# Kernel tuning notes

Hardware: AMD Instinct MI355X
Metric: run time of the kernel (lower is better)

The kernel has to match this reference:

```python
import jax, jax.numpy as jnp
import numpy as np

N_NODES = 100000
N_EDGES = 1600000
IN_F = 64
OUT_F = 40
K_HOPS = 3
N_CLUSTERS = 10000


def setup_inputs() -> dict:
    key = jax.random.key(0)
    k1, k2, k3, k4 = jax.random.split(key, 4)
    x = jax.random.normal(k1, (N_NODES, IN_F), dtype=jnp.float32)
    edge_index = jax.random.randint(k2, (2, N_EDGES), 0, N_NODES, dtype=jnp.int32)
    cluster_index = jax.random.randint(k3, (N_NODES,), 0, N_CLUSTERS, dtype=jnp.int32)
    W = jax.random.normal(k4, (OUT_F, IN_F), dtype=jnp.float32) * (1.0 / np.sqrt(IN_F))
    b = jnp.zeros((OUT_F,), dtype=jnp.float32)
    return {"x": x, "edge_index": edge_index, "cluster_index": cluster_index,
            "num_clusters": N_CLUSTERS, "W": W, "b": b}


def reference(x, edge_index, cluster_index, num_clusters, W, b):
    N = x.shape[0]
    self_loop = jnp.arange(N, dtype=edge_index.dtype)
    row = jnp.concatenate([edge_index[0], self_loop])  # target nodes
    col = jnp.concatenate([edge_index[1], self_loop])  # source nodes
    ones = jnp.ones(row.shape[0], dtype=x.dtype)
    deg = jax.ops.segment_sum(ones, row, num_segments=N)
    dinv = jax.lax.rsqrt(jnp.maximum(deg, 1.0))
    norm = dinv[row] * dinv[col]  # [E+N] symmetric GCN normalization
    # K-hop propagation: x <- D^{-1/2} (A+I) D^{-1/2} x, K times
    for _ in range(K_HOPS):
        x = jax.ops.segment_sum(x[col] * norm[:, None], row, num_segments=N)
    # cluster/compress: segment-mean of node features per cluster -> [C, F]
    cnt = jax.ops.segment_sum(jnp.ones(N, dtype=x.dtype), cluster_index,
                              num_segments=num_clusters)
    xc = jax.ops.segment_sum(x, cluster_index, num_segments=num_clusters)
    xc = xc / jnp.maximum(cnt, 1.0)[:, None]
    # dense linear on compressed rows, then reconstruct (gather back)
    h = xc @ W.T + b  # [C, OUT_F]
    out = h[cluster_index]  # [N, OUT_F]
    # original module computes log_softmax into a local `out` but returns x
    return out
```

## Files before the change

### kernel.cpp

```cpp
#include <hip/hip_runtime.h>

#define N_NODES    100000
#define N_EDGES    1600000
#define IN_F       64
#define OUT_F      40
#define N_CLUSTERS 10000

#define BUCK_SHIFT 7
#define BROWS      128
#define NBUCK      ((N_NODES + BROWS - 1) >> BUCK_SHIFT)
#define CAP        2560
#define TILE_E     4096
#define EPT        (TILE_E / 256)

typedef _Float16 half_t;
typedef _Float16 half4_t __attribute__((ext_vector_type(4)));

__global__ __launch_bounds__(256) void bin_scatter_kernel(
        const int* __restrict__ rows, const int* __restrict__ cols,
        int* __restrict__ bcursor, unsigned* __restrict__ bins) {
    __shared__ uint2 se[TILE_E];
    __shared__ int lh[NBUCK];
    __shared__ int lsc[NBUCK];
    __shared__ int lb[NBUCK];
    __shared__ int sc[256];
    int t = threadIdx.x;
    for (int i = t; i < NBUCK; i += 256) lh[i] = 0;
    __syncthreads();
    int e0 = blockIdx.x * TILE_E;
    int r[EPT], c[EPT], rk[EPT];
    #pragma unroll
    for (int k = 0; k < EPT; ++k) {
        int e = e0 + t + k * 256;
        if (e < N_EDGES) {
            r[k] = rows[e]; c[k] = cols[e];
            rk[k] = atomicAdd(&lh[r[k] >> BUCK_SHIFT], 1);
        } else r[k] = -1;
    }
    __syncthreads();
    int b4 = t * 4;
    int a0 = (b4 + 0 < NBUCK) ? lh[b4 + 0] : 0;
    int a1 = (b4 + 1 < NBUCK) ? lh[b4 + 1] : 0;
    int a2 = (b4 + 2 < NBUCK) ? lh[b4 + 2] : 0;
    int a3 = (b4 + 3 < NBUCK) ? lh[b4 + 3] : 0;
    int thr = a0 + a1 + a2 + a3;
    sc[t] = thr;
    __syncthreads();
    for (int off = 1; off < 256; off <<= 1) {
        int a = (t >= off) ? sc[t - off] : 0;
        __syncthreads();
        sc[t] += a;
        __syncthreads();
    }
    int ex = sc[t] - thr;
    if (b4 + 0 < NBUCK) { lsc[b4 + 0] = ex;                lb[b4 + 0] = a0 ? atomicAdd(&bcursor[b4 + 0], a0) : 0; }
    if (b4 + 1 < NBUCK) { lsc[b4 + 1] = ex + a0;           lb[b4 + 1] = a1 ? atomicAdd(&bcursor[b4 + 1], a1) : 0; }
    if (b4 + 2 < NBUCK) { lsc[b4 + 2] = ex + a0 + a1;      lb[b4 + 2] = a2 ? atomicAdd(&bcursor[b4 + 2], a2) : 0; }
    if (b4 + 3 < NBUCK) { lsc[b4 + 3] = ex + a0 + a1 + a2; lb[b4 + 3] = a3 ? atomicAdd(&bcursor[b4 + 3], a3) : 0; }
    __syncthreads();
    #pragma unroll
    for (int k = 0; k < EPT; ++k) {
        if (r[k] >= 0) {
            int bu = r[k] >> BUCK_SHIFT;
            se[lsc[bu] + rk[k]] = make_uint2((unsigned)r[k], (unsigned)c[k]);
        }
    }
    __syncthreads();
    #pragma unroll
    for (int k = 0; k < EPT; ++k) {
        int idx = k * 256 + t;
        if (e0 + idx < N_EDGES) {
            uint2 u = se[idx];
            int bu = (int)(u.x >> BUCK_SHIFT);
            int pos = lb[bu] + (idx - lsc[bu]);
            if (pos < CAP)
                bins[(size_t)bu * CAP + pos] = ((u.x & (BROWS - 1)) << 17) | u.y;
        }
    }
}

__global__ __launch_bounds__(256) void csr_build_kernel(
        const unsigned* __restrict__ bins, const int* __restrict__ bcnt,
        int* __restrict__ csr_col, uint2* __restrict__ rowinfo,
        float* __restrict__ dinv, const int* __restrict__ cl,
        int* __restrict__ ccnt) {
    __shared__ int lcnt[BROWS];
    __shared__ int gbeg[BROWS];
    __shared__ int sc[BROWS];
    int b = blockIdx.x, t = threadIdx.x;
    int n = min(bcnt[b], CAP);
    const unsigned* eb = bins + (size_t)b * CAP;
    if (t < BROWS) lcnt[t] = 0;
    __syncthreads();
    for (int i = t; i < n; i += 256) atomicAdd(&lcnt[eb[i] >> 17], 1);
    __syncthreads();
    int v = (t < BROWS) ? lcnt[t] : 0;
    if (t < BROWS) sc[t] = v;
    __syncthreads();
    for (int off = 1; off < BROWS; off <<= 1) {
        int a = (t >= off && t < BROWS) ? sc[t - off] : 0;
        __syncthreads();
        if (t < BROWS) sc[t] += a;
        __syncthreads();
    }
    if (t < BROWS) {
        int beg = b * CAP + sc[t] - v;
        gbeg[t] = beg;
        int grow = (b << BUCK_SHIFT) + t;
        if (grow < N_NODES) {
            rowinfo[grow] = make_uint2((unsigned)beg, (unsigned)v);
            dinv[grow] = rsqrtf((float)(v + 1));
            atomicAdd(&ccnt[cl[grow]], 1);
        }
        lcnt[t] = 0;
    }
    __syncthreads();
    for (int i = t; i < n; i += 256) {
        unsigned u = eb[i];
        int lrow = (int)(u >> 17);
        int pos = atomicAdd(&lcnt[lrow], 1);
        csr_col[gbeg[lrow] + pos] = (int)(u & 0x1FFFFu);
    }
}

__global__ __launch_bounds__(256, 8) void prologue_kernel(
        const float4* __restrict__ x4, const float* __restrict__ W,
        const float* __restrict__ dinv, half_t* __restrict__ z0) {
    __shared__ float Ws[OUT_F * 65];
    int t = threadIdx.x;
    for (int i = t; i < OUT_F * IN_F; i += 256)
        Ws[(i >> 6) * 65 + (i & 63)] = W[i];
    __syncthreads();
    int idx = blockIdx.x * 256 + t;
    if (idx >= N_NODES * OUT_F) return;
    int node = idx / OUT_F;
    int o = idx - node * OUT_F;
    const float4* xr = x4 + node * 16;
    const float* wr = Ws + o * 65;
    float acc = 0.f;
    #pragma unroll
    for (int k4 = 0; k4 < 16; ++k4) {
        float4 v = xr[k4];
        acc += v.x * wr[k4 * 4 + 0] + v.y * wr[k4 * 4 + 1]
             + v.z * wr[k4 * 4 + 2] + v.w * wr[k4 * 4 + 3];
    }
    z0[idx] = (half_t)(acc * dinv[node]);
}

template<int FINAL>
__global__ __launch_bounds__(256, 8) void hop40_kernel(
        const half_t* __restrict__ zin, half_t* __restrict__ zout,
        const uint2* __restrict__ rowinfo, const int* __restrict__ csr_col,
        const float* __restrict__ dinv, const int* __restrict__ cl,
        float* __restrict__ xc) {
    __shared__ half4_t srow[160];
    int t = threadIdx.x;
    int w = t >> 6;
    int lane = t & 63;
    int slot = lane / 10;
    int ql = lane - slot * 10;
    int slotj = (slot < 6) ? slot : 1000;
    int nb = blockIdx.x << 4;
    #pragma unroll
    for (int i = 0; i < 4; ++i) {
        int node = nb + (w << 2) + i;
        uint2 ri = rowinfo[node];
        int beg = (int)ri.x;
        int end = beg + (int)ri.y;
        float4 acc = make_float4(0.f, 0.f, 0.f, 0.f);
        if (slot == 0) {
            half4_t v = ((const half4_t*)(zin + (size_t)node * OUT_F))[ql];
            acc.x = (float)v.x; acc.y = (float)v.y; acc.z = (float)v.z; acc.w = (float)v.w;
        }
        for (int base = beg; base < end; base += 64) {
            int idx = base + lane;
            int cv = (idx < end) ? csr_col[idx] : 0;
            int lim = min(64, end - base);
            int gmax = (lim + 23) / 24;
            for (int g = 0; g < gmax; ++g) {
                int j0 = g * 24 + slotj;
                int c0 = __shfl(cv, (j0     ) & 63);
                int c1 = __shfl(cv, (j0 +  6) & 63);
                int c2 = __shfl(cv, (j0 + 12) & 63);
                int c3 = __shfl(cv, (j0 + 18) & 63);
                half4_t v0 = ((const half4_t*)(zin + (size_t)c0 * OUT_F))[ql];
                half4_t v1 = ((const half4_t*)(zin + (size_t)c1 * OUT_F))[ql];
                half4_t v2 = ((const half4_t*)(zin + (size_t)c2 * OUT_F))[ql];
                half4_t v3 = ((const half4_t*)(zin + (size_t)c3 * OUT_F))[ql];
                float m0 = (j0      < lim) ? 1.f : 0.f;
                float m1 = (j0 +  6 < lim) ? 1.f : 0.f;
                float m2 = (j0 + 12 < lim) ? 1.f : 0.f;
                float m3 = (j0 + 18 < lim) ? 1.f : 0.f;
                acc.x += m0 * (float)v0.x; acc.y += m0 * (float)v0.y;
                acc.z += m0 * (float)v0.z; acc.w += m0 * (float)v0.w;
                acc.x += m1 * (float)v1.x; acc.y += m1 * (float)v1.y;
                acc.z += m1 * (float)v1.z; acc.w += m1 * (float)v1.w;
                acc.x += m2 * (float)v2.x; acc.y += m2 * (float)v2.y;
                acc.z += m2 * (float)v2.z; acc.w += m2 * (float)v2.w;
                acc.x += m3 * (float)v3.x; acc.y += m3 * (float)v3.y;
                acc.z += m3 * (float)v3.z; acc.w += m3 * (float)v3.w;
            }
        }
        float4 t1;
        t1.x = __shfl(acc.x, (lane + 30) & 63); t1.y = __shfl(acc.y, (lane + 30) & 63);
        t1.z = __shfl(acc.z, (lane + 30) & 63); t1.w = __shfl(acc.w, (lane + 30) & 63);
        if (lane < 30) { acc.x += t1.x; acc.y += t1.y; acc.z += t1.z; acc.w += t1.w; }
        float4 t2, t3;
        t2.x = __shfl(acc.x, (lane + 10) & 63); t2.y = __shfl(acc.y, (lane + 10) & 63);
        t2.z = __shfl(acc.z, (lane + 10) & 63); t2.w = __shfl(acc.w, (lane + 10) & 63);
        t3.x = __shfl(acc.x, (lane + 20) & 63); t3.y = __shfl(acc.y, (lane + 20) & 63);
        t3.z = __shfl(acc.z, (lane + 20) & 63); t3.w = __shfl(acc.w, (lane + 20) & 63);
        if (lane < 10) {
            acc.x += t2.x + t3.x; acc.y += t2.y + t3.y;
            acc.z += t2.z + t3.z; acc.w += t2.w + t3.w;
            float d = dinv[node];
            if (FINAL) {
                float* p = xc + cl[node] * OUT_F + ql * 4;
                atomicAdd(p + 0, acc.x * d); atomicAdd(p + 1, acc.y * d);
                atomicAdd(p + 2, acc.z * d); atomicAdd(p + 3, acc.w * d);
            } else {
                float s = d * d;
                half4_t o;
                o.x = (half_t)(acc.x * s); o.y = (half_t)(acc.y * s);
                o.z = (half_t)(acc.z * s); o.w = (half_t)(acc.w * s);
                srow[((w << 2) + i) * 10 + ql] = o;
            }
        }
    }
    if (!FINAL) {
        __syncthreads();
        if (t < 160) ((half4_t*)zout)[(size_t)blockIdx.x * 160 + t] = srow[t];
    }
}

__global__ void epilogue_kernel(const float4* __restrict__ xc4, const int* __restrict__ ccnt,
                                const float4* __restrict__ b4, const int* __restrict__ cl,
                                float4* __restrict__ out4) {
    int i = blockIdx.x * 256 + threadIdx.x;
    if (i >= N_NODES * (OUT_F / 4)) return;
    int node = i / 10;
    int q = i - node * 10;
    int c = cl[node];
    float inv = 1.0f / fmaxf((float)ccnt[c], 1.0f);
    float4 v = xc4[c * 10 + q];
    float4 bb = b4[q];
    v.x = v.x * inv + bb.x; v.y = v.y * inv + bb.y;
    v.z = v.z * inv + bb.z; v.w = v.w * inv + bb.w;
    out4[i] = v;
}

extern "C" void kernel_launch(void* const* d_in, const int* in_sizes, int n_in,
                              void* d_out, int out_size, void* d_ws, size_t ws_size,
                              hipStream_t stream) {
    const float* x    = (const float*)d_in[0];
    const int*   rows = (const int*)d_in[1];
    const int*   cols = (const int*)d_in[1] + N_EDGES;
    const int*   cl   = (const int*)d_in[2];
    const float* W    = (const float*)d_in[4];
    const float* b    = (const float*)d_in[5];
    float* out = (float*)d_out;

    size_t off = 0;
    auto alloc = [&](size_t elems) -> void* {
        void* p = (char*)d_ws + off * 4;
        off += (elems + 63) & ~(size_t)63;
        return p;
    };
    int*   ccnt    = (int*)alloc(N_CLUSTERS);
    float* xc_sum  = (float*)alloc((size_t)N_CLUSTERS * OUT_F);
    int*   bcursor = (int*)alloc(NBUCK);
    size_t zero_elems = off;
    float* dinv      = (float*)alloc(N_NODES);
    uint2* rowinfo   = (uint2*)alloc((size_t)N_NODES * 2);
    int*   csr_col   = (int*)alloc((size_t)NBUCK * CAP);
    unsigned* bins   = (unsigned*)alloc((size_t)NBUCK * CAP);
    half_t* bufA     = (half_t*)alloc((size_t)N_NODES * OUT_F / 2);
    half_t* bufB     = (half_t*)alloc((size_t)N_NODES * OUT_F / 2);
    (void)ws_size; (void)in_sizes; (void)n_in; (void)out_size;

    hipMemsetAsync(d_ws, 0, zero_elems * 4, stream);

    const int TB = (N_EDGES + TILE_E - 1) / TILE_E;
    const int HB = N_NODES / 16;

    bin_scatter_kernel<<<TB, 256, 0, stream>>>(rows, cols, bcursor, bins);
    csr_build_kernel<<<NBUCK, 256, 0, stream>>>(bins, bcursor, csr_col, rowinfo,
                                                dinv, cl, ccnt);

    prologue_kernel<<<(N_NODES * OUT_F + 255) / 256, 256, 0, stream>>>(
        (const float4*)x, W, dinv, bufA);

    hop40_kernel<0><<<HB, 256, 0, stream>>>(bufA, bufB, rowinfo, csr_col, dinv, cl, xc_sum);
    hop40_kernel<0><<<HB, 256, 0, stream>>>(bufB, bufA, rowinfo, csr_col, dinv, cl, xc_sum);
    hop40_kernel<1><<<HB, 256, 0, stream>>>(bufA, (half_t*)nullptr, rowinfo, csr_col, dinv, cl, xc_sum);

    epilogue_kernel<<<(N_NODES * (OUT_F / 4) + 255) / 256, 256, 0, stream>>>(
        (const float4*)xc_sum, ccnt, (const float4*)b, cl, (float4*)out);
}
```

Baseline: 335.5 us.

## Split 40-wide features into two 20-wide halves propagated separately

The feature matrix is stored as two separate 20-column fp16 arrays, and the three-hop propagation runs twice, once per half. The goal is a 2MB working set per hop that fits better in L2/MALL for the random gathers, and 12 edges processed in parallel per wavefront instead of 6. The cost is launching six hop kernels instead of three, reading the CSR twice as often, and a deeper shuffle reduction. Column indices are now loaded with nontemporal hints.

After: 457.8 us. 1.36x slower.

```diff
diff --git a/kernel.cpp b/kernel.cpp
--- a/kernel.cpp
+++ b/kernel.cpp
@@ -125,7 +125,8 @@
 
 __global__ __launch_bounds__(256, 8) void prologue_kernel(
         const float4* __restrict__ x4, const float* __restrict__ W,
-        const float* __restrict__ dinv, half_t* __restrict__ z0) {
+        const float* __restrict__ dinv, half_t* __restrict__ zlo,
+        half_t* __restrict__ zhi) {
     __shared__ float Ws[OUT_F * 65];
     int t = threadIdx.x;
     for (int i = t; i < OUT_F * IN_F; i += 256)
@@ -144,22 +145,24 @@
         acc += v.x * wr[k4 * 4 + 0] + v.y * wr[k4 * 4 + 1]
              + v.z * wr[k4 * 4 + 2] + v.w * wr[k4 * 4 + 3];
     }
-    z0[idx] = (half_t)(acc * dinv[node]);
+    half_t h = (half_t)(acc * dinv[node]);
+    if (o < 20) zlo[node * 20 + o]      = h;
+    else        zhi[node * 20 + o - 20] = h;
 }
 
 template<int FINAL>
-__global__ __launch_bounds__(256, 8) void hop40_kernel(
+__global__ __launch_bounds__(256, 8) void hop20_kernel(
         const half_t* __restrict__ zin, half_t* __restrict__ zout,
         const uint2* __restrict__ rowinfo, const int* __restrict__ csr_col,
         const float* __restrict__ dinv, const int* __restrict__ cl,
-        float* __restrict__ xc) {
-    __shared__ half4_t srow[160];
+        float* __restrict__ xc, int dbase) {
+    __shared__ half4_t srow[80];
     int t = threadIdx.x;
     int w = t >> 6;
     int lane = t & 63;
-    int slot = lane / 10;
-    int ql = lane - slot * 10;
-    int slotj = (slot < 6) ? slot : 1000;
+    int slot = lane / 5;
+    int ql = lane - slot * 5;
+    int slotj = (slot < 12) ? slot : 1000;
     int nb = blockIdx.x << 4;
     #pragma unroll
     for (int i = 0; i < 4; ++i) {
@@ -169,28 +172,28 @@
         int end = beg + (int)ri.y;
         float4 acc = make_float4(0.f, 0.f, 0.f, 0.f);
         if (slot == 0) {
-            half4_t v = ((const half4_t*)(zin + (size_t)node * OUT_F))[ql];
+            half4_t v = ((const half4_t*)(zin + (size_t)node * 20))[ql];
             acc.x = (float)v.x; acc.y = (float)v.y; acc.z = (float)v.z; acc.w = (float)v.w;
         }
         for (int base = beg; base < end; base += 64) {
             int idx = base + lane;
-            int cv = (idx < end) ? csr_col[idx] : 0;
+            int cv = (idx < end) ? __builtin_nontemporal_load(csr_col + idx) : 0;
             int lim = min(64, end - base);
-            int gmax = (lim + 23) / 24;
+            int gmax = (lim + 47) / 48;
             for (int g = 0; g < gmax; ++g) {
-                int j0 = g * 24 + slotj;
+                int j0 = g * 48 + slotj;
                 int c0 = __shfl(cv, (j0     ) & 63);
-                int c1 = __shfl(cv, (j0 +  6) & 63);
-                int c2 = __shfl(cv, (j0 + 12) & 63);
-                int c3 = __shfl(cv, (j0 + 18) & 63);
-                half4_t v0 = ((const half4_t*)(zin + (size_t)c0 * OUT_F))[ql];
-                half4_t v1 = ((const half4_t*)(zin + (size_t)c1 * OUT_F))[ql];
-                half4_t v2 = ((const half4_t*)(zin + (size_t)c2 * OUT_F))[ql];
-                half4_t v3 = ((const half4_t*)(zin + (size_t)c3 * OUT_F))[ql];
+                int c1 = __shfl(cv, (j0 + 12) & 63);
+                int c2 = __shfl(cv, (j0 + 24) & 63);
+                int c3 = __shfl(cv, (j0 + 36) & 63);
+                half4_t v0 = ((const half4_t*)(zin + (size_t)c0 * 20))[ql];
+                half4_t v1 = ((const half4_t*)(zin + (size_t)c1 * 20))[ql];
+                half4_t v2 = ((const half4_t*)(zin + (size_t)c2 * 20))[ql];
+                half4_t v3 = ((const half4_t*)(zin + (size_t)c3 * 20))[ql];
                 float m0 = (j0      < lim) ? 1.f : 0.f;
-                float m1 = (j0 +  6 < lim) ? 1.f : 0.f;
-                float m2 = (j0 + 12 < lim) ? 1.f : 0.f;
-                float m3 = (j0 + 18 < lim) ? 1.f : 0.f;
+                float m1 = (j0 + 12 < lim) ? 1.f : 0.f;
+                float m2 = (j0 + 24 < lim) ? 1.f : 0.f;
+                float m3 = (j0 + 36 < lim) ? 1.f : 0.f;
                 acc.x += m0 * (float)v0.x; acc.y += m0 * (float)v0.y;
                 acc.z += m0 * (float)v0.z; acc.w += m0 * (float)v0.w;
                 acc.x += m1 * (float)v1.x; acc.y += m1 * (float)v1.y;
@@ -205,17 +208,21 @@
         t1.x = __shfl(acc.x, (lane + 30) & 63); t1.y = __shfl(acc.y, (lane + 30) & 63);
         t1.z = __shfl(acc.z, (lane + 30) & 63); t1.w = __shfl(acc.w, (lane + 30) & 63);
         if (lane < 30) { acc.x += t1.x; acc.y += t1.y; acc.z += t1.z; acc.w += t1.w; }
-        float4 t2, t3;
-        t2.x = __shfl(acc.x, (lane + 10) & 63); t2.y = __shfl(acc.y, (lane + 10) & 63);
-        t2.z = __shfl(acc.z, (lane + 10) & 63); t2.w = __shfl(acc.w, (lane + 10) & 63);
-        t3.x = __shfl(acc.x, (lane + 20) & 63); t3.y = __shfl(acc.y, (lane + 20) & 63);
-        t3.z = __shfl(acc.z, (lane + 20) & 63); t3.w = __shfl(acc.w, (lane + 20) & 63);
-        if (lane < 10) {
-            acc.x += t2.x + t3.x; acc.y += t2.y + t3.y;
-            acc.z += t2.z + t3.z; acc.w += t2.w + t3.w;
+        float4 t2;
+        t2.x = __shfl(acc.x, (lane + 15) & 63); t2.y = __shfl(acc.y, (lane + 15) & 63);
+        t2.z = __shfl(acc.z, (lane + 15) & 63); t2.w = __shfl(acc.w, (lane + 15) & 63);
+        if (lane < 15) { acc.x += t2.x; acc.y += t2.y; acc.z += t2.z; acc.w += t2.w; }
+        float4 t3, t4;
+        t3.x = __shfl(acc.x, (lane + 5) & 63);  t3.y = __shfl(acc.y, (lane + 5) & 63);
+        t3.z = __shfl(acc.z, (lane + 5) & 63);  t3.w = __shfl(acc.w, (lane + 5) & 63);
+        t4.x = __shfl(acc.x, (lane + 10) & 63); t4.y = __shfl(acc.y, (lane + 10) & 63);
+        t4.z = __shfl(acc.z, (lane + 10) & 63); t4.w = __shfl(acc.w, (lane + 10) & 63);
+        if (lane < 5) {
+            acc.x += t3.x + t4.x; acc.y += t3.y + t4.y;
+            acc.z += t3.z + t4.z; acc.w += t3.w + t4.w;
             float d = dinv[node];
             if (FINAL) {
-                float* p = xc + cl[node] * OUT_F + ql * 4;
+                float* p = xc + cl[node] * OUT_F + dbase + lane * 4;
                 atomicAdd(p + 0, acc.x * d); atomicAdd(p + 1, acc.y * d);
                 atomicAdd(p + 2, acc.z * d); atomicAdd(p + 3, acc.w * d);
             } else {
@@ -223,13 +230,13 @@
                 half4_t o;
                 o.x = (half_t)(acc.x * s); o.y = (half_t)(acc.y * s);
                 o.z = (half_t)(acc.z * s); o.w = (half_t)(acc.w * s);
-                srow[((w << 2) + i) * 10 + ql] = o;
+                srow[((w << 2) + i) * 5 + lane] = o;
             }
         }
     }
     if (!FINAL) {
         __syncthreads();
-        if (t < 160) ((half4_t*)zout)[(size_t)blockIdx.x * 160 + t] = srow[t];
+        if (t < 80) ((half4_t*)zout)[(size_t)blockIdx.x * 80 + t] = srow[t];
     }
 }
 
@@ -274,8 +281,10 @@
     uint2* rowinfo   = (uint2*)alloc((size_t)N_NODES * 2);
     int*   csr_col   = (int*)alloc((size_t)NBUCK * CAP);
     unsigned* bins   = (unsigned*)alloc((size_t)NBUCK * CAP);
-    half_t* bufA     = (half_t*)alloc((size_t)N_NODES * OUT_F / 2);
-    half_t* bufB     = (half_t*)alloc((size_t)N_NODES * OUT_F / 2);
+    half_t* bufAlo   = (half_t*)alloc((size_t)N_NODES * 10);
+    half_t* bufAhi   = (half_t*)alloc((size_t)N_NODES * 10);
+    half_t* bufBlo   = (half_t*)alloc((size_t)N_NODES * 10);
+    half_t* bufBhi   = (half_t*)alloc((size_t)N_NODES * 10);
     (void)ws_size; (void)in_sizes; (void)n_in; (void)out_size;
 
     hipMemsetAsync(d_ws, 0, zero_elems * 4, stream);
@@ -288,11 +297,14 @@
                                                 dinv, cl, ccnt);
 
     prologue_kernel<<<(N_NODES * OUT_F + 255) / 256, 256, 0, stream>>>(
-        (const float4*)x, W, dinv, bufA);
-
-    hop40_kernel<0><<<HB, 256, 0, stream>>>(bufA, bufB, rowinfo, csr_col, dinv, cl, xc_sum);
-    hop40_kernel<0><<<HB, 256, 0, stream>>>(bufB, bufA, rowinfo, csr_col, dinv, cl, xc_sum);
-    hop40_kernel<1><<<HB, 256, 0, stream>>>(bufA, (half_t*)nullptr, rowinfo, csr_col, dinv, cl, xc_sum);
+        (const float4*)x, W, dinv, bufAlo, bufAhi);
+
+    hop20_kernel<0><<<HB, 256, 0, stream>>>(bufAlo, bufBlo, rowinfo, csr_col, dinv, cl, xc_sum, 0);
+    hop20_kernel<0><<<HB, 256, 0, stream>>>(bufBlo, bufAlo, rowinfo, csr_col, dinv, cl, xc_sum, 0);
+    hop20_kernel<1><<<HB, 256, 0, stream>>>(bufAlo, (half_t*)nullptr, rowinfo, csr_col, dinv, cl, xc_sum, 0);
+    hop20_kernel<0><<<HB, 256, 0, stream>>>(bufAhi, bufBhi, rowinfo, csr_col, dinv, cl, xc_sum, 20);
+    hop20_kernel<0><<<HB, 256, 0, stream>>>(bufBhi, bufAhi, rowinfo, csr_col, dinv, cl, xc_sum, 20);
+    hop20_kernel<1><<<HB, 256, 0, stream>>>(bufAhi, (half_t*)nullptr, rowinfo, csr_col, dinv, cl, xc_sum, 20);
 
     epilogue_kernel<<<(N_NODES * (OUT_F / 4) + 255) / 256, 256, 0, stream>>>(
         (const float4*)xc_sum, ccnt, (const float4*)b, cl, (float4*)out);
```
